# Kernel optimization log

Hardware: AMD Instinct MI355X
Metric: run time of the kernel (lower is better)

Reference implementation:

```python
import jax, jax.numpy as jnp
import numpy as np

N = 50000
E = 1600000
IN_C = 64
HID = 16
HEADS = 4
OUT_C = 1
ATT_SLOPE = 0.2   # GATConv negative_slope for attention logits
ACT_SLOPE = 0.01  # F.leaky_relu default between layers


def _glorot(key, shape):
    fan_in, fan_out = shape[0], shape[-1]
    lim = jnp.sqrt(6.0 / (fan_in + fan_out))
    return jax.random.uniform(key, shape, jnp.float32, -lim, lim)


def setup_inputs() -> dict:
    key = jax.random.key(0)
    ks = jax.random.split(key, 12)
    x = jax.random.normal(ks[0], (N, IN_C), jnp.float32)
    edge_index = jax.random.randint(ks[1], (2, E), 0, N, jnp.int64)
    return {
        "x": x,
        "edge_index": edge_index,
        # GAT layer 1: in -> HID per head, HEADS heads (concat)
        "W1": _glorot(ks[2], (IN_C, HEADS * HID)),
        "att_src1": _glorot(ks[3], (HEADS, HID)),
        "att_dst1": _glorot(ks[4], (HEADS, HID)),
        "b1": jnp.zeros((HEADS * HID,), jnp.float32),
        # GAT layer 2: HEADS*HID -> HID, 1 head
        "W2": _glorot(ks[5], (HEADS * HID, HID)),
        "att_src2": _glorot(ks[6], (1, HID)),
        "att_dst2": _glorot(ks[7], (1, HID)),
        "b2": jnp.zeros((HID,), jnp.float32),
        # final linear
        "Wo": _glorot(ks[8], (HID, OUT_C)),
        "bo": jnp.zeros((OUT_C,), jnp.float32),
    }


def _gat_layer(x, src, dst, W, a_src, a_dst, b, n_nodes):
    """PyG GATConv (eval mode): h = xW; edge logits from additive attention;
    segment softmax over incoming edges of each dst; weighted scatter-sum."""
    H, C = a_src.shape
    h = (x @ W).reshape(n_nodes, H, C)                       # [N, H, C]
    alpha_s = jnp.einsum("nhc,hc->nh", h, a_src)             # [N, H]
    alpha_d = jnp.einsum("nhc,hc->nh", h, a_dst)             # [N, H]
    e = jax.nn.leaky_relu(alpha_s[src] + alpha_d[dst], ATT_SLOPE)  # [E, H]
    m = jax.ops.segment_max(e, dst, num_segments=n_nodes)    # [N, H]
    w = jnp.exp(e - m[dst])
    denom = jax.ops.segment_sum(w, dst, num_segments=n_nodes)
    alpha = w / denom[dst]                                   # [E, H] (self-loops => denom>0)
    out = jax.ops.segment_sum(h[src] * alpha[:, :, None], dst, num_segments=n_nodes)
    return out.reshape(n_nodes, H * C) + b                   # concat heads + bias


def reference(x, edge_index, W1, att_src1, att_dst1, b1,
              W2, att_src2, att_dst2, b2, Wo, bo):
    n = x.shape[0]
    loops = jnp.arange(n, dtype=edge_index.dtype)
    src = jnp.concatenate([edge_index[0], loops])            # add_self_loops=True
    dst = jnp.concatenate([edge_index[1], loops])
    h = _gat_layer(x, src, dst, W1, att_src1, att_dst1, b1, n)
    h = jax.nn.leaky_relu(h, ACT_SLOPE)
    h = _gat_layer(h, src, dst, W2, att_src2, att_dst2, b2, n)
    h = jax.nn.leaky_relu(h, ACT_SLOPE)
    return h @ Wo + bo                                       # [N, 1]
```

## Files before the change

### kernel.cpp

```cpp
#include <hip/hip_runtime.h>
#include <hip/hip_bf16.h>
#include <cstdint>

#define N_NODES 50000
#define N_EDGES 1600000
#define EE (N_EDGES + N_NODES)
#define BSH 7
#define BSIZE 128
#define NBUCKET ((N_NODES + BSIZE - 1) >> BSH)
#define CSH 13
#define CAP 8192
#define BIN_BLOCKS 403
#define GEMM_BLOCKS 3125

__device__ __forceinline__ float lrelu(float x, float s) { return x >= 0.f ? x : s * x; }
__device__ __forceinline__ float bflo(uint32_t v) { return __uint_as_float(v << 16); }
__device__ __forceinline__ float bfhi(uint32_t v) { return __uint_as_float(v & 0xFFFF0000u); }
__device__ __forceinline__ uint32_t bfpackhi(float a) {
    uint32_t u = __float_as_uint(a);
    u += 0x7FFF + ((u >> 16) & 1);
    return u & 0xFFFF0000u;
}
__device__ __forceinline__ uint32_t packbf(float a, float b) {
    uint32_t ua = __float_as_uint(a), ub = __float_as_uint(b);
    ua += 0x7FFF + ((ua >> 16) & 1);
    ub += 0x7FFF + ((ub >> 16) & 1);
    return (ua >> 16) | (ub & 0xFFFF0000u);
}
__device__ __forceinline__ float rdlane(float v, int l) {
    return __uint_as_float(__builtin_amdgcn_readlane(__float_as_uint(v), l));
}

__global__ __launch_bounds__(256) void k_pre(
    const float* __restrict__ x, const float* __restrict__ W1,
    const float* __restrict__ as_w, const float* __restrict__ ad_w,
    uint32_t* __restrict__ h1b, float* __restrict__ as1, float* __restrict__ ad1,
    const int* __restrict__ src, const int* __restrict__ dst,
    int* __restrict__ bcur, uint32_t* __restrict__ binned) {
    if (blockIdx.x < BIN_BLOCKS) {
        __shared__ int lcnt[NBUCKET];
        __shared__ int lbase[NBUCKET];
        const int T = 16;
        for (int i = threadIdx.x; i < NBUCKET; i += 256) lcnt[i] = 0;
        __syncthreads();
        uint32_t pv[T];
        uint32_t pm[T];
        int base = blockIdx.x * (256 * T);
#pragma unroll
        for (int k = 0; k < T; k++) {
            int e = base + k * 256 + threadIdx.x;
            if (e < EE) {
                int s, d;
                if (e < N_EDGES) { s = src[e]; d = dst[e]; } else { s = e - N_EDGES; d = s; }
                int b = d >> BSH;
                int r = atomicAdd(&lcnt[b], 1);
                pv[k] = (uint32_t)s | ((uint32_t)(d & (BSIZE - 1)) << 16);
                pm[k] = (uint32_t)r | ((uint32_t)b << 16);
            }
        }
        __syncthreads();
        for (int i = threadIdx.x; i < NBUCKET; i += 256) {
            int c = lcnt[i];
            if (c) lbase[i] = atomicAdd(&bcur[i], c);
        }
        __syncthreads();
#pragma unroll
        for (int k = 0; k < T; k++) {
            int e = base + k * 256 + threadIdx.x;
            if (e < EE) {
                int b = pm[k] >> 16, r = pm[k] & 0xFFFF;
                binned[((size_t)b << CSH) + lbase[b] + r] = pv[k];
            }
        }
        return;
    }
    int c = threadIdx.x & 63;
    int wv = threadIdx.x >> 6;
    float wreg[64];
#pragma unroll
    for (int k = 0; k < 64; k++) wreg[k] = W1[k * 64 + c];
    float aw = as_w[c];
    float dw = ad_w[c];
    int base = (blockIdx.x - BIN_BLOCKS) * 16 + wv * 4;
#pragma unroll
    for (int r = 0; r < 4; r++) {
        int n = base + r;
        float xr = x[n * 64 + c];
        float a0 = 0.f, a1 = 0.f, a2 = 0.f, a3 = 0.f;
#pragma unroll
        for (int k = 0; k < 64; k += 4) {
            a0 = fmaf(rdlane(xr, k),     wreg[k],     a0);
            a1 = fmaf(rdlane(xr, k + 1), wreg[k + 1], a1);
            a2 = fmaf(rdlane(xr, k + 2), wreg[k + 2], a2);
            a3 = fmaf(rdlane(xr, k + 3), wreg[k + 3], a3);
        }
        float acc = (a0 + a1) + (a2 + a3);
        float other = __shfl_xor(acc, 1, 64);
        if (!(c & 1)) h1b[n * 32 + (c >> 1)] = packbf(acc, other);
        float asv = acc * aw;
        float adv = acc * dw;
#pragma unroll
        for (int off = 1; off < 16; off <<= 1) {
            asv += __shfl_xor(asv, off, 64);
            adv += __shfl_xor(adv, off, 64);
        }
        if ((c & 15) == 0) { as1[n * 4 + (c >> 4)] = asv; ad1[n * 4 + (c >> 4)] = adv; }
    }
}

__global__ __launch_bounds__(512) void kB_sort(const int* __restrict__ bcur, const uint32_t* __restrict__ binned,
                                               const float* __restrict__ as1, const float* __restrict__ ad1,
                                               int* __restrict__ rowdesc, uint32_t* __restrict__ sbn,
                                               uint32_t* __restrict__ wbuf) {
    int b = blockIdx.x, tid = threadIdx.x, wv = tid >> 6;
    int p0 = b << CSH;
    int L = bcur[b];
    __shared__ int cnt8[8][BSIZE];
    __shared__ int wbase[8][BSIZE];
    __shared__ int shs[BSIZE];
    for (int i = tid; i < 8 * BSIZE; i += 512) ((int*)cnt8)[i] = 0;
    __syncthreads();

    uint32_t pv[16];
    unsigned short rk[16];
#pragma unroll
    for (int k = 0; k < 16; k++) {
        int i = tid + k * 512;
        if (i < L) {
            uint32_t v = binned[p0 + i];
            pv[k] = v;
            rk[k] = (unsigned short)atomicAdd(&cnt8[wv][(v >> 16) & (BSIZE - 1)], 1);
        }
    }
    __syncthreads();

    int tot = 0;
    if (tid < BSIZE) {
#pragma unroll
        for (int w = 0; w < 8; w++) tot += cnt8[w][tid];
        shs[tid] = tot;
    }
    __syncthreads();
    for (int off = 1; off < BSIZE; off <<= 1) {
        int t = 0;
        if (tid < BSIZE && tid >= off) t = shs[tid - off];
        __syncthreads();
        if (tid < BSIZE && tid >= off) shs[tid] += t;
        __syncthreads();
    }
    if (tid < BSIZE) {
        int excl = shs[tid] - tot;
        int node = (b << BSH) + tid;
        if (node < N_NODES) rowdesc[node] = excl | (tot << 13);
        int wb = excl;
#pragma unroll
        for (int w = 0; w < 8; w++) { wbase[w][tid] = wb; wb += cnt8[w][tid]; }
    }
    __syncthreads();

#pragma unroll
    for (int k = 0; k < 16; k++) {
        int i = tid + k * 512;
        if (i < L) {
            uint32_t v = pv[k];
            int dl = (v >> 16) & (BSIZE - 1);
            int s = (int)(v & 0xFFFF);
            int pos = wbase[wv][dl] + (int)rk[k];
            int node = (b << BSH) + dl;
            float4 a = *(const float4*)(as1 + s * 4);
            float4 d = *(const float4*)(ad1 + node * 4);
            float e0 = a.x + d.x, e1 = a.y + d.y, e2 = a.z + d.z, e3 = a.w + d.w;
            float w0 = __expf(e0 >= 0.f ? e0 : 0.2f * e0);
            float w1 = __expf(e1 >= 0.f ? e1 : 0.2f * e1);
            float w2 = __expf(e2 >= 0.f ? e2 : 0.2f * e2);
            float w3 = __expf(e3 >= 0.f ? e3 : 0.2f * e3);
            sbn[p0 + pos] = (uint32_t)s | ((uint32_t)dl << 16);
            wbuf[(size_t)(p0 + pos) * 2]     = packbf(w0, w1);
            wbuf[(size_t)(p0 + pos) * 2 + 1] = packbf(w2, w3);
        }
    }
}

__global__ __launch_bounds__(256) void k_aggr1f(
    const int* __restrict__ rowdesc, const uint32_t* __restrict__ sbn,
    const uint32_t* __restrict__ wbuf, const uint32_t* __restrict__ h1b,
    const float* __restrict__ b1, const float* __restrict__ W2,
    const float* __restrict__ as2w, const float* __restrict__ ad2w,
    float* __restrict__ h2, float* __restrict__ as2, float* __restrict__ ad2) {
    int n = blockIdx.x * 4 + (threadIdx.x >> 6);
    int lane = threadIdx.x & 63;
    int md = rowdesc[n];
    int begin = ((n >> BSH) << CSH) + (md & (CAP - 1));
    int deg = md >> 13;

    int slot = lane >> 3, cl = lane & 7;
    int hc = cl >> 1;
    int wsel = hc >> 1, whalf = hc & 1;

    const uint4* h1b4 = (const uint4*)h1b;
    float a0 = 0.f, a1 = 0.f, a2 = 0.f, a3 = 0.f, a4 = 0.f, a5 = 0.f, a6 = 0.f, a7 = 0.f, dsum = 0.f;

    int iters = (deg + 7) >> 3;
#pragma unroll 4
    for (int it = 0; it < iters; it++) {
        int idx = it * 8 + slot;
        uint32_t sv = sbn[begin + idx];
        uint32_t wp = wbuf[(size_t)(begin + idx) * 2 + wsel];
        float w = whalf ? bfhi(wp) : bflo(wp);
        w = (idx < deg) ? w : 0.f;
        int s = (int)(sv & 0xFFFF);
        uint4 v = h1b4[s * 8 + cl];
        dsum += w;
        a0 += w * bflo(v.x); a1 += w * bfhi(v.x);
        a2 += w * bflo(v.y); a3 += w * bfhi(v.y);
        a4 += w * bflo(v.z); a5 += w * bfhi(v.z);
        a6 += w * bflo(v.w); a7 += w * bfhi(v.w);
    }
#pragma unroll
    for (int off = 8; off <= 32; off <<= 1) {
        a0 += __shfl_xor(a0, off, 64); a1 += __shfl_xor(a1, off, 64);
        a2 += __shfl_xor(a2, off, 64); a3 += __shfl_xor(a3, off, 64);
        a4 += __shfl_xor(a4, off, 64); a5 += __shfl_xor(a5, off, 64);
        a6 += __shfl_xor(a6, off, 64); a7 += __shfl_xor(a7, off, 64);
        dsum += __shfl_xor(dsum, off, 64);
    }
    float dinv = 1.f / dsum;

    float4 bb0 = *(const float4*)(b1 + 8 * cl);
    float4 bb1 = *(const float4*)(b1 + 8 * cl + 4);
    float act0 = lrelu(a0 * dinv + bb0.x, 0.01f);
    float act1 = lrelu(a1 * dinv + bb0.y, 0.01f);
    float act2 = lrelu(a2 * dinv + bb0.z, 0.01f);
    float act3 = lrelu(a3 * dinv + bb0.w, 0.01f);
    float act4 = lrelu(a4 * dinv + bb1.x, 0.01f);
    float act5 = lrelu(a5 * dinv + bb1.y, 0.01f);
    float act6 = lrelu(a6 * dinv + bb1.z, 0.01f);
    float act7 = lrelu(a7 * dinv + bb1.w, 0.01f);

    int co = lane & 15, kg = lane >> 4;
    int l0 = 2 * kg, l1 = 2 * kg + 1;
    const float* w2r = W2 + (16 * kg) * 16 + co;
    float g = 0.f;
    g = fmaf(__shfl(act0, l0, 64), w2r[0 * 16],  g);
    g = fmaf(__shfl(act1, l0, 64), w2r[1 * 16],  g);
    g = fmaf(__shfl(act2, l0, 64), w2r[2 * 16],  g);
    g = fmaf(__shfl(act3, l0, 64), w2r[3 * 16],  g);
    g = fmaf(__shfl(act4, l0, 64), w2r[4 * 16],  g);
    g = fmaf(__shfl(act5, l0, 64), w2r[5 * 16],  g);
    g = fmaf(__shfl(act6, l0, 64), w2r[6 * 16],  g);
    g = fmaf(__shfl(act7, l0, 64), w2r[7 * 16],  g);
    g = fmaf(__shfl(act0, l1, 64), w2r[8 * 16],  g);
    g = fmaf(__shfl(act1, l1, 64), w2r[9 * 16],  g);
    g = fmaf(__shfl(act2, l1, 64), w2r[10 * 16], g);
    g = fmaf(__shfl(act3, l1, 64), w2r[11 * 16], g);
    g = fmaf(__shfl(act4, l1, 64), w2r[12 * 16], g);
    g = fmaf(__shfl(act5, l1, 64), w2r[13 * 16], g);
    g = fmaf(__shfl(act6, l1, 64), w2r[14 * 16], g);
    g = fmaf(__shfl(act7, l1, 64), w2r[15 * 16], g);
    g += __shfl_xor(g, 16, 64);
    g += __shfl_xor(g, 32, 64);
    if (lane < 16) h2[n * 16 + co] = g;
    float asv = g * as2w[co];
    float adv2 = g * ad2w[co];
#pragma unroll
    for (int off = 1; off < 16; off <<= 1) {
        asv += __shfl_xor(asv, off, 64);
        adv2 += __shfl_xor(adv2, off, 64);
    }
    if (lane == 0) { as2[n] = asv; ad2[n] = adv2; }
}

__global__ __launch_bounds__(256) void k_w2(
    const int* __restrict__ bcur, const uint32_t* __restrict__ sbn,
    const float* __restrict__ as2, const float* __restrict__ ad2,
    uint32_t* __restrict__ earr2) {
    int slot = blockIdx.x * 256 + threadIdx.x;
    int b = slot >> CSH, i = slot & (CAP - 1);
    if (i >= bcur[b]) return;
    uint32_t v = sbn[slot];
    int s = (int)(v & 0xFFFF);
    int node = (b << BSH) + (int)(v >> 16);
    float e = as2[s] + ad2[node];
    float w = __expf(e >= 0.f ? e : 0.2f * e);
    earr2[slot] = bfpackhi(w) | (uint32_t)s;
}

__global__ __launch_bounds__(256) void k_aggr2(
    const int* __restrict__ rowdesc, const uint32_t* __restrict__ earr2,
    const float* __restrict__ h2,
    const float* __restrict__ b2, const float* __restrict__ Wo,
    const float* __restrict__ bo, float* __restrict__ out) {
    int n = blockIdx.x * 4 + (threadIdx.x >> 6);
    int lane = threadIdx.x & 63;
    int md = rowdesc[n];
    int begin = ((n >> BSH) << CSH) + (md & (CAP - 1));
    int deg = md >> 13;

    int slot = lane >> 3, c2 = lane & 7;
    const float2* h22 = (const float2*)h2;
    float acc0 = 0.f, acc1 = 0.f, dsum = 0.f;

    int iters = (deg + 7) >> 3;
#pragma unroll 4
    for (int it = 0; it < iters; it++) {
        int idx = it * 8 + slot;
        uint32_t ewd = earr2[begin + idx];
        float w = __uint_as_float(ewd & 0xFFFF0000u);
        w = (idx < deg) ? w : 0.f;
        int s = (int)(ewd & 0xFFFF);
        float2 hv = h22[s * 8 + c2];
        acc0 += w * hv.x;
        acc1 += w * hv.y;
        dsum += w;
    }
#pragma unroll
    for (int off = 8; off <= 32; off <<= 1) {
        acc0 += __shfl_xor(acc0, off, 64);
        acc1 += __shfl_xor(acc1, off, 64);
        dsum += __shfl_xor(dsum, off, 64);
    }
    float v0 = lrelu(acc0 / dsum + b2[2 * c2], 0.01f) * Wo[2 * c2];
    float v1 = lrelu(acc1 / dsum + b2[2 * c2 + 1], 0.01f) * Wo[2 * c2 + 1];
    float y = v0 + v1;
    y += __shfl_xor(y, 1, 64);
    y += __shfl_xor(y, 2, 64);
    y += __shfl_xor(y, 4, 64);
    if (lane == 0) out[n] = y + bo[0];
}

extern "C" void kernel_launch(void* const* d_in, const int* in_sizes, int n_in,
                              void* d_out, int out_size, void* d_ws, size_t ws_size,
                              hipStream_t stream) {
    const float* x    = (const float*)d_in[0];
    const int*   ei   = (const int*)d_in[1];
    const float* W1   = (const float*)d_in[2];
    const float* as1w = (const float*)d_in[3];
    const float* ad1w = (const float*)d_in[4];
    const float* b1   = (const float*)d_in[5];
    const float* W2   = (const float*)d_in[6];
    const float* as2w = (const float*)d_in[7];
    const float* ad2w = (const float*)d_in[8];
    const float* b2   = (const float*)d_in[9];
    const float* Wo   = (const float*)d_in[10];
    const float* bo   = (const float*)d_in[11];
    float* out = (float*)d_out;

    const int* srcp = ei;
    const int* dstp = ei + N_EDGES;

    char* p = (char*)d_ws;
    auto alloc = [&](size_t bytes) -> char* {
        char* r = p;
        p += (bytes + 255) / 256 * 256;
        return r;
    };
    int*      bcur    = (int*)alloc((size_t)(NBUCKET + 1) * 4);
    int*      rowdesc = (int*)alloc((size_t)N_NODES * 4);
    uint32_t* binned  = (uint32_t*)alloc((size_t)NBUCKET * CAP * 4);
    uint32_t* sbn     = (uint32_t*)alloc((size_t)NBUCKET * CAP * 4 + 256);
    uint32_t* wbuf    = (uint32_t*)alloc((size_t)NBUCKET * CAP * 8 + 256);
    uint32_t* earr2   = (uint32_t*)alloc((size_t)NBUCKET * CAP * 4 + 256);
    float*    h2      = (float*)alloc((size_t)N_NODES * 16 * 4);
    uint32_t* h1b     = (uint32_t*)alloc((size_t)N_NODES * 32 * 4);
    float*    as1     = (float*)alloc((size_t)N_NODES * 4 * 4);
    float*    ad1     = (float*)alloc((size_t)N_NODES * 4 * 4);
    float*    as2     = (float*)alloc((size_t)N_NODES * 4);
    float*    ad2     = (float*)alloc((size_t)N_NODES * 4);
    (void)alloc(3 * 1024 * 1024);

    hipMemsetAsync(bcur, 0, (size_t)(NBUCKET + 1) * 4, stream);

    k_pre<<<BIN_BLOCKS + GEMM_BLOCKS, 256, 0, stream>>>(x, W1, as1w, ad1w, h1b, as1, ad1,
                                                        srcp, dstp, bcur, binned);
    kB_sort<<<NBUCKET, 512, 0, stream>>>(bcur, binned, as1, ad1, rowdesc, sbn, wbuf);
    k_aggr1f<<<N_NODES / 4, 256, 0, stream>>>(rowdesc, sbn, wbuf, h1b, b1, W2, as2w, ad2w, h2, as2, ad2);
    k_w2<<<NBUCKET * (CAP / 256), 256, 0, stream>>>(bcur, sbn, as2, ad2, earr2);
    k_aggr2<<<N_NODES / 4, 256, 0, stream>>>(rowdesc, earr2, h2, b2, Wo, bo, out);
}
```

Baseline: 218.9 us.

## Compute edge attention weights inline in aggregation kernels, drop weight buffers

The sort kernel now writes only a compact 16-bit source index per edge, instead of precomputing and storing the layer-1 edge weights in bf16. Both aggregation kernels recompute the leaky-relu and exp logits from the per-node as/ad arrays while gathering. The separate layer-2 weight kernel and its buffer are removed. The GEMM in k_pre also swaps readlane broadcasts for direct float4 loads of each x row. This cuts edge-array memory traffic and one launch, in exchange for extra random gathers of as1/as2 and exp work inside the aggregation loops.

```diff
diff --git a/kernel.cpp b/kernel.cpp
--- a/kernel.cpp
+++ b/kernel.cpp
@@ -16,19 +16,11 @@
 __device__ __forceinline__ float lrelu(float x, float s) { return x >= 0.f ? x : s * x; }
 __device__ __forceinline__ float bflo(uint32_t v) { return __uint_as_float(v << 16); }
 __device__ __forceinline__ float bfhi(uint32_t v) { return __uint_as_float(v & 0xFFFF0000u); }
-__device__ __forceinline__ uint32_t bfpackhi(float a) {
-    uint32_t u = __float_as_uint(a);
-    u += 0x7FFF + ((u >> 16) & 1);
-    return u & 0xFFFF0000u;
-}
 __device__ __forceinline__ uint32_t packbf(float a, float b) {
     uint32_t ua = __float_as_uint(a), ub = __float_as_uint(b);
     ua += 0x7FFF + ((ua >> 16) & 1);
     ub += 0x7FFF + ((ub >> 16) & 1);
     return (ua >> 16) | (ub & 0xFFFF0000u);
-}
-__device__ __forceinline__ float rdlane(float v, int l) {
-    return __uint_as_float(__builtin_amdgcn_readlane(__float_as_uint(v), l));
 }
 
 __global__ __launch_bounds__(256) void k_pre(
@@ -85,16 +77,17 @@
 #pragma unroll
     for (int r = 0; r < 4; r++) {
         int n = base + r;
-        float xr = x[n * 64 + c];
-        float a0 = 0.f, a1 = 0.f, a2 = 0.f, a3 = 0.f;
-#pragma unroll
-        for (int k = 0; k < 64; k += 4) {
-            a0 = fmaf(rdlane(xr, k),     wreg[k],     a0);
-            a1 = fmaf(rdlane(xr, k + 1), wreg[k + 1], a1);
-            a2 = fmaf(rdlane(xr, k + 2), wreg[k + 2], a2);
-            a3 = fmaf(rdlane(xr, k + 3), wreg[k + 3], a3);
-        }
-        float acc = (a0 + a1) + (a2 + a3);
+        const float4* xr4 = (const float4*)(x + (size_t)n * 64);
+        float A0 = 0.f, A1 = 0.f, A2 = 0.f, A3 = 0.f;
+#pragma unroll
+        for (int k4 = 0; k4 < 16; k4++) {
+            float4 xv = xr4[k4];
+            A0 = fmaf(xv.x, wreg[4 * k4 + 0], A0);
+            A1 = fmaf(xv.y, wreg[4 * k4 + 1], A1);
+            A2 = fmaf(xv.z, wreg[4 * k4 + 2], A2);
+            A3 = fmaf(xv.w, wreg[4 * k4 + 3], A3);
+        }
+        float acc = (A0 + A1) + (A2 + A3);
         float other = __shfl_xor(acc, 1, 64);
         if (!(c & 1)) h1b[n * 32 + (c >> 1)] = packbf(acc, other);
         float asv = acc * aw;
@@ -109,9 +102,7 @@
 }
 
 __global__ __launch_bounds__(512) void kB_sort(const int* __restrict__ bcur, const uint32_t* __restrict__ binned,
-                                               const float* __restrict__ as1, const float* __restrict__ ad1,
-                                               int* __restrict__ rowdesc, uint32_t* __restrict__ sbn,
-                                               uint32_t* __restrict__ wbuf) {
+                                               int* __restrict__ rowdesc, unsigned short* __restrict__ esrc) {
     int b = blockIdx.x, tid = threadIdx.x, wv = tid >> 6;
     int p0 = b << CSH;
     int L = bcur[b];
@@ -164,26 +155,15 @@
         if (i < L) {
             uint32_t v = pv[k];
             int dl = (v >> 16) & (BSIZE - 1);
-            int s = (int)(v & 0xFFFF);
-            int pos = wbase[wv][dl] + (int)rk[k];
-            int node = (b << BSH) + dl;
-            float4 a = *(const float4*)(as1 + s * 4);
-            float4 d = *(const float4*)(ad1 + node * 4);
-            float e0 = a.x + d.x, e1 = a.y + d.y, e2 = a.z + d.z, e3 = a.w + d.w;
-            float w0 = __expf(e0 >= 0.f ? e0 : 0.2f * e0);
-            float w1 = __expf(e1 >= 0.f ? e1 : 0.2f * e1);
-            float w2 = __expf(e2 >= 0.f ? e2 : 0.2f * e2);
-            float w3 = __expf(e3 >= 0.f ? e3 : 0.2f * e3);
-            sbn[p0 + pos] = (uint32_t)s | ((uint32_t)dl << 16);
-            wbuf[(size_t)(p0 + pos) * 2]     = packbf(w0, w1);
-            wbuf[(size_t)(p0 + pos) * 2 + 1] = packbf(w2, w3);
+            esrc[p0 + wbase[wv][dl] + (int)rk[k]] = (unsigned short)(v & 0xFFFF);
         }
     }
 }
 
 __global__ __launch_bounds__(256) void k_aggr1f(
-    const int* __restrict__ rowdesc, const uint32_t* __restrict__ sbn,
-    const uint32_t* __restrict__ wbuf, const uint32_t* __restrict__ h1b,
+    const int* __restrict__ rowdesc, const unsigned short* __restrict__ esrc,
+    const float* __restrict__ as1, const float* __restrict__ ad1,
+    const uint32_t* __restrict__ h1b,
     const float* __restrict__ b1, const float* __restrict__ W2,
     const float* __restrict__ as2w, const float* __restrict__ ad2w,
     float* __restrict__ h2, float* __restrict__ as2, float* __restrict__ ad2) {
@@ -195,7 +175,7 @@
 
     int slot = lane >> 3, cl = lane & 7;
     int hc = cl >> 1;
-    int wsel = hc >> 1, whalf = hc & 1;
+    float ad1h = ad1[n * 4 + hc];
 
     const uint4* h1b4 = (const uint4*)h1b;
     float a0 = 0.f, a1 = 0.f, a2 = 0.f, a3 = 0.f, a4 = 0.f, a5 = 0.f, a6 = 0.f, a7 = 0.f, dsum = 0.f;
@@ -204,11 +184,10 @@
 #pragma unroll 4
     for (int it = 0; it < iters; it++) {
         int idx = it * 8 + slot;
-        uint32_t sv = sbn[begin + idx];
-        uint32_t wp = wbuf[(size_t)(begin + idx) * 2 + wsel];
-        float w = whalf ? bfhi(wp) : bflo(wp);
+        int s = esrc[begin + idx];
+        float e = as1[s * 4 + hc] + ad1h;
+        float w = __expf(e >= 0.f ? e : 0.2f * e);
         w = (idx < deg) ? w : 0.f;
-        int s = (int)(sv & 0xFFFF);
         uint4 v = h1b4[s * 8 + cl];
         dsum += w;
         a0 += w * bflo(v.x); a1 += w * bfhi(v.x);
@@ -270,23 +249,9 @@
     if (lane == 0) { as2[n] = asv; ad2[n] = adv2; }
 }
 
-__global__ __launch_bounds__(256) void k_w2(
-    const int* __restrict__ bcur, const uint32_t* __restrict__ sbn,
+__global__ __launch_bounds__(256) void k_aggr2(
+    const int* __restrict__ rowdesc, const unsigned short* __restrict__ esrc,
     const float* __restrict__ as2, const float* __restrict__ ad2,
-    uint32_t* __restrict__ earr2) {
-    int slot = blockIdx.x * 256 + threadIdx.x;
-    int b = slot >> CSH, i = slot & (CAP - 1);
-    if (i >= bcur[b]) return;
-    uint32_t v = sbn[slot];
-    int s = (int)(v & 0xFFFF);
-    int node = (b << BSH) + (int)(v >> 16);
-    float e = as2[s] + ad2[node];
-    float w = __expf(e >= 0.f ? e : 0.2f * e);
-    earr2[slot] = bfpackhi(w) | (uint32_t)s;
-}
-
-__global__ __launch_bounds__(256) void k_aggr2(
-    const int* __restrict__ rowdesc, const uint32_t* __restrict__ earr2,
     const float* __restrict__ h2,
     const float* __restrict__ b2, const float* __restrict__ Wo,
     const float* __restrict__ bo, float* __restrict__ out) {
@@ -295,6 +260,7 @@
     int md = rowdesc[n];
     int begin = ((n >> BSH) << CSH) + (md & (CAP - 1));
     int deg = md >> 13;
+    float adv = ad2[n];
 
     int slot = lane >> 3, c2 = lane & 7;
     const float2* h22 = (const float2*)h2;
@@ -304,10 +270,10 @@
 #pragma unroll 4
     for (int it = 0; it < iters; it++) {
         int idx = it * 8 + slot;
-        uint32_t ewd = earr2[begin + idx];
-        float w = __uint_as_float(ewd & 0xFFFF0000u);
+        int s = esrc[begin + idx];
+        float e = as2[s] + adv;
+        float w = __expf(e >= 0.f ? e : 0.2f * e);
         w = (idx < deg) ? w : 0.f;
-        int s = (int)(ewd & 0xFFFF);
         float2 hv = h22[s * 8 + c2];
         acc0 += w * hv.x;
         acc1 += w * hv.y;
@@ -354,26 +320,23 @@
         p += (bytes + 255) / 256 * 256;
         return r;
     };
-    int*      bcur    = (int*)alloc((size_t)(NBUCKET + 1) * 4);
-    int*      rowdesc = (int*)alloc((size_t)N_NODES * 4);
-    uint32_t* binned  = (uint32_t*)alloc((size_t)NBUCKET * CAP * 4);
-    uint32_t* sbn     = (uint32_t*)alloc((size_t)NBUCKET * CAP * 4 + 256);
-    uint32_t* wbuf    = (uint32_t*)alloc((size_t)NBUCKET * CAP * 8 + 256);
-    uint32_t* earr2   = (uint32_t*)alloc((size_t)NBUCKET * CAP * 4 + 256);
-    float*    h2      = (float*)alloc((size_t)N_NODES * 16 * 4);
-    uint32_t* h1b     = (uint32_t*)alloc((size_t)N_NODES * 32 * 4);
-    float*    as1     = (float*)alloc((size_t)N_NODES * 4 * 4);
-    float*    ad1     = (float*)alloc((size_t)N_NODES * 4 * 4);
-    float*    as2     = (float*)alloc((size_t)N_NODES * 4);
-    float*    ad2     = (float*)alloc((size_t)N_NODES * 4);
-    (void)alloc(3 * 1024 * 1024);
+    int*            bcur    = (int*)alloc((size_t)(NBUCKET + 1) * 4);
+    int*            rowdesc = (int*)alloc((size_t)N_NODES * 4);
+    uint32_t*       binned  = (uint32_t*)alloc((size_t)NBUCKET * CAP * 4);
+    unsigned short* esrc    = (unsigned short*)alloc((size_t)NBUCKET * CAP * 2 + 256);
+    float*          h2      = (float*)alloc((size_t)N_NODES * 16 * 4);
+    uint32_t*       h1b     = (uint32_t*)alloc((size_t)N_NODES * 32 * 4);
+    float*          as1     = (float*)alloc((size_t)N_NODES * 4 * 4);
+    float*          ad1     = (float*)alloc((size_t)N_NODES * 4 * 4);
+    float*          as2     = (float*)alloc((size_t)N_NODES * 4);
+    float*          ad2     = (float*)alloc((size_t)N_NODES * 4);
+    (void)alloc(4 * 1024 * 1024);
 
     hipMemsetAsync(bcur, 0, (size_t)(NBUCKET + 1) * 4, stream);
 
     k_pre<<<BIN_BLOCKS + GEMM_BLOCKS, 256, 0, stream>>>(x, W1, as1w, ad1w, h1b, as1, ad1,
                                                         srcp, dstp, bcur, binned);
-    kB_sort<<<NBUCKET, 512, 0, stream>>>(bcur, binned, as1, ad1, rowdesc, sbn, wbuf);
-    k_aggr1f<<<N_NODES / 4, 256, 0, stream>>>(rowdesc, sbn, wbuf, h1b, b1, W2, as2w, ad2w, h2, as2, ad2);
-    k_w2<<<NBUCKET * (CAP / 256), 256, 0, stream>>>(bcur, sbn, as2, ad2, earr2);
-    k_aggr2<<<N_NODES / 4, 256, 0, stream>>>(rowdesc, earr2, h2, b2, Wo, bo, out);
-}
+    kB_sort<<<NBUCKET, 512, 0, stream>>>(bcur, binned, rowdesc, esrc);
+    k_aggr1f<<<N_NODES / 4, 256, 0, stream>>>(rowdesc, esrc, as1, ad1, h1b, b1, W2, as2w, ad2w, h2, as2, ad2);
+    k_aggr2<<<N_NODES / 4, 256, 0, stream>>>(rowdesc, esrc, as2, ad2, h2, b2, Wo, bo, out);
+}
```

Result: faster. 208.3 us (-4.8%).
